# Performance work log

Hardware: AMD Instinct MI355X
Metric: run time of the kernel (lower is better)

The kernel has to match this reference:

```python
import jax, jax.numpy as jnp
import numpy as np

# Multi-scale deformable attention (MSDeformableAttention from RTDETRTransformerv2)
SPATIAL = ((80, 80), (40, 40), (20, 20))  # (h, w) per level, strides 8/16/32 on 640x640
N_HEADS, N_LEVELS, N_POINTS = 8, 3, 4
D_MODEL = 256
HEAD_DIM = D_MODEL // N_HEADS


def setup_inputs() -> dict:
    key = jax.random.key(0)
    ks = jax.random.split(key, 10)
    B, Q = 16, 300
    Lv = sum(h * w for h, w in SPATIAL)  # 8400
    s = 0.02
    return {
        "query": jax.random.normal(ks[0], (B, Q, D_MODEL), jnp.float32),
        "reference_points": jax.random.uniform(ks[1], (B, Q, 4), jnp.float32),
        "value": jax.random.normal(ks[2], (B, Lv, D_MODEL), jnp.float32),
        "Wv": jax.random.normal(ks[3], (D_MODEL, D_MODEL), jnp.float32) * s,
        "bv": jnp.zeros((D_MODEL,), jnp.float32),
        "Woff": jax.random.normal(ks[4], (D_MODEL, N_HEADS * N_LEVELS * N_POINTS * 2), jnp.float32) * s,
        "boff": jax.random.normal(ks[5], (N_HEADS * N_LEVELS * N_POINTS * 2,), jnp.float32) * 0.1,
        "Wattn": jax.random.normal(ks[6], (D_MODEL, N_HEADS * N_LEVELS * N_POINTS), jnp.float32) * s,
        "battn": jnp.zeros((N_HEADS * N_LEVELS * N_POINTS,), jnp.float32),
        "Wout": jax.random.normal(ks[7], (D_MODEL, D_MODEL), jnp.float32) * s,
        "bout": jnp.zeros((D_MODEL,), jnp.float32),
    }


def _grid_sample_level(v_lvl, gx, gy, h, w):
    """Bilinear grid_sample, align_corners=False, zeros padding.

    v_lvl : (B, nH, h*w, hd) flattened per-level value map
    gx,gy : (B, nH, P) sample coords in [-1, 1]
    returns (B, nH, P, hd)
    """
    px = ((gx + 1.0) * w - 1.0) * 0.5  # pixel x
    py = ((gy + 1.0) * h - 1.0) * 0.5  # pixel y
    x0 = jnp.floor(px)
    y0 = jnp.floor(py)
    fx = px - x0
    fy = py - y0
    x0i = x0.astype(jnp.int32)
    y0i = y0.astype(jnp.int32)

    def corner(xi, yi, wgt):
        valid = (xi >= 0) & (xi < w) & (yi >= 0) & (yi < h)
        idx = jnp.clip(yi, 0, h - 1) * w + jnp.clip(xi, 0, w - 1)
        g = jnp.take_along_axis(v_lvl, idx[..., None], axis=2)  # (B,nH,P,hd)
        return g * (wgt * valid.astype(wgt.dtype))[..., None]

    return (corner(x0i, y0i, (1 - fx) * (1 - fy))
            + corner(x0i + 1, y0i, fx * (1 - fy))
            + corner(x0i, y0i + 1, (1 - fx) * fy)
            + corner(x0i + 1, y0i + 1, fx * fy))


def reference(query, reference_points, value, Wv, bv, Woff, boff, Wattn, battn, Wout, bout):
    B, Q, _ = query.shape
    # value projection -> per-head values
    v = (value @ Wv + bv).reshape(B, -1, N_HEADS, HEAD_DIM)
    # sampling offsets and attention weights from queries
    off = (query @ Woff + boff).reshape(B, Q, N_HEADS, N_LEVELS, N_POINTS, 2)
    aw = jax.nn.softmax(
        (query @ Wattn + battn).reshape(B, Q, N_HEADS, N_LEVELS * N_POINTS), axis=-1
    ).reshape(B, Q, N_HEADS, N_LEVELS, N_POINTS)
    # reference points (cx, cy) broadcast over heads/levels/points
    ref = reference_points[:, :, None, None, None, :2]
    pts = jnp.clip(ref + off, 0.0, 1.0)      # (B,Q,nH,nL,nP,2) in [0,1]
    g = pts * 2.0 - 1.0                      # grid_sample coords in [-1,1]

    out = jnp.zeros((B, Q, N_HEADS, HEAD_DIM), query.dtype)
    start = 0
    for lvl, (h, w) in enumerate(SPATIAL):
        v_lvl = v[:, start:start + h * w].transpose(0, 2, 1, 3)  # (B,nH,hw,hd)
        gl = g[:, :, :, lvl]                                     # (B,Q,nH,nP,2)
        gx = gl[..., 0].transpose(0, 2, 1, 3).reshape(B, N_HEADS, Q * N_POINTS)
        gy = gl[..., 1].transpose(0, 2, 1, 3).reshape(B, N_HEADS, Q * N_POINTS)
        sampled = _grid_sample_level(v_lvl, gx, gy, h, w)        # (B,nH,Q*nP,hd)
        sampled = sampled.reshape(B, N_HEADS, Q, N_POINTS, HEAD_DIM)
        wl = aw[:, :, :, lvl].transpose(0, 2, 1, 3)              # (B,nH,Q,nP)
        out = out + jnp.einsum('bhqpd,bhqp->bqhd', sampled, wl)
        start += h * w

    return out.reshape(B, Q, D_MODEL) @ Wout + bout
```

## Files before the change

kernel.cpp:

```cpp
#include <hip/hip_runtime.h>
#include <hip/hip_bf16.h>
#include <cstddef>

#define NB 16
#define NQ 300
#define DM 256
#define LV_ 8400

typedef __attribute__((ext_vector_type(8))) short short8;
typedef __attribute__((ext_vector_type(4))) float f32x4;

static __device__ __forceinline__ unsigned short bf16_rne(float f) {
  unsigned int u = __builtin_bit_cast(unsigned int, f);
  u += 0x7FFFu + ((u >> 16) & 1u);
  return (unsigned short)(u >> 16);
}

static __device__ __forceinline__ unsigned int pack_bf2(float a, float b) {
  __hip_bfloat162 p = __float22bfloat162_rn(make_float2(a, b));
  unsigned int u;
  __builtin_memcpy(&u, &p, 4);
  return u;
}

static __device__ __forceinline__ void gload16(const void* g, void* l) {
  __builtin_amdgcn_global_load_lds(
      (const __attribute__((address_space(1))) unsigned int*)g,
      (__attribute__((address_space(3))) unsigned int*)l, 16, 0, 0);
}

__global__ __launch_bounds__(256) void prep_kernel(
    const float* __restrict__ Wv, const float* __restrict__ Wout,
    unsigned short* __restrict__ WthP, unsigned short* __restrict__ WoutT) {
  __shared__ float tle[32][33];
  const int k0 = blockIdx.x * 32, n0 = blockIdx.y * 32;
  const int xx = threadIdx.x & 31, y4 = (threadIdx.x >> 5) * 4;
  const float* src = blockIdx.z ? Wout : Wv;
  #pragma unroll
  for (int i = 0; i < 4; ++i)
    tle[y4 + i][xx] = src[(size_t)(k0 + y4 + i) * DM + n0 + xx];
  __syncthreads();
  if (blockIdx.z == 0) {
    if (threadIdx.x < 128) {
      const int nl = threadIdx.x >> 2, q8 = threadIdx.x & 3;
      const int n = n0 + nl, yy = n >> 7, col = n & 127;
      uint4 o;
      o.x = pack_bf2(tle[q8 * 8 + 0][nl], tle[q8 * 8 + 1][nl]);
      o.y = pack_bf2(tle[q8 * 8 + 2][nl], tle[q8 * 8 + 3][nl]);
      o.z = pack_bf2(tle[q8 * 8 + 4][nl], tle[q8 * 8 + 5][nl]);
      o.w = pack_bf2(tle[q8 * 8 + 6][nl], tle[q8 * 8 + 7][nl]);
      const size_t idx = ((((size_t)yy * 8 + blockIdx.x) * 4 + q8) * 128 + col) * 8;
      *(uint4*)&WthP[idx] = o;
    }
  } else {
    #pragma unroll
    for (int i = 0; i < 4; ++i)
      WoutT[(size_t)(n0 + y4 + i) * DM + k0 + xx] = bf16_rne(tle[xx][y4 + i]);
  }
}

__global__ __launch_bounds__(256, 3) void vproj_mfma(
    const float* __restrict__ A, const unsigned short* __restrict__ WthP,
    const float* __restrict__ bias, unsigned short* __restrict__ V) {
  __shared__ float Af[2][128][32];
  __shared__ unsigned short Bf[2][4][128][8];
  const int tid = threadIdx.x;
  const int lane = tid & 63;
  const int wave = tid >> 6;
  const int l16 = lane & 15, q4 = lane >> 4;
  const int wr = (wave >> 1) * 64, wc = (wave & 1) * 64;

  const int b = blockIdx.x;
  const int xcd = b & 7, cidx = b >> 3;
  const int w = (xcd < 4 ? xcd * 263 : 4 * 263 + (xcd - 4) * 262) + cidx;
  const int xb = w >> 1, y = w & 1;
  const size_t row0 = (size_t)xb * 128;
  const int col0 = y * 128;

  const unsigned short* bsrc = WthP + (size_t)y * 8 * 4096;

#define STAGE(bufi, kb_) do {                                                  \
    _Pragma("unroll")                                                          \
    for (int c_ = 0; c_ < 4; ++c_) {                                           \
      const int u_ = wave * 4 + c_;                                            \
      const int row_ = u_ * 8 + (lane >> 3);                                   \
      const int lu_ = (lane & 7) ^ (row_ & 7);                                 \
      gload16(A + (row0 + row_) * DM + (kb_) * 32 + lu_ * 4,                   \
              (char*)&Af[bufi][0][0] + u_ * 1024);                             \
    }                                                                          \
    _Pragma("unroll")                                                          \
    for (int c_ = 0; c_ < 2; ++c_) {                                           \
      const int u_ = wave * 2 + c_;                                            \
      gload16(bsrc + (size_t)(kb_) * 4096 + u_ * 512 + lane * 8,               \
              (char*)&Bf[bufi][0][0][0] + u_ * 1024);                          \
    }                                                                          \
  } while (0)

  f32x4 acc[4][4];
  #pragma unroll
  for (int i = 0; i < 4; ++i)
    #pragma unroll
    for (int j = 0; j < 4; ++j) acc[i][j] = (f32x4)0.f;

  int buf = 0;
  STAGE(0, 0);
  __syncthreads();

  for (int kb = 0; kb < 8; ++kb) {
    if (kb < 7) STAGE(buf ^ 1, kb + 1);

    short8 bfr[4];
    #pragma unroll
    for (int j = 0; j < 4; ++j)
      bfr[j] = *(const short8*)&Bf[buf][q4][wc + j * 16 + l16][0];

    #pragma unroll
    for (int i = 0; i < 4; ++i) {
      const int r_ = wr + i * 16 + l16;
      const float* rp = &Af[buf][r_][0];
      const int sw = (r_ & 7);
      const float4 lo = *(const float4*)(rp + ((((q4 << 1) + 0) ^ sw) << 2));
      const float4 hi = *(const float4*)(rp + ((((q4 << 1) + 1) ^ sw) << 2));
      uint4 p;
      p.x = pack_bf2(lo.x, lo.y); p.y = pack_bf2(lo.z, lo.w);
      p.z = pack_bf2(hi.x, hi.y); p.w = pack_bf2(hi.z, hi.w);
      const short8 af = __builtin_bit_cast(short8, p);
      #pragma unroll
      for (int j = 0; j < 4; ++j)
        acc[i][j] = __builtin_amdgcn_mfma_f32_16x16x32_bf16(af, bfr[j], acc[i][j], 0, 0, 0);
    }
    __syncthreads();
    buf ^= 1;
  }
#undef STAGE

  #pragma unroll
  for (int i = 0; i < 4; ++i)
    #pragma unroll
    for (int j = 0; j < 4; ++j) {
      const int col = col0 + wc + j * 16 + l16;
      const float bcol = bias[col];
      #pragma unroll
      for (int r = 0; r < 4; ++r) {
        const size_t row = row0 + wr + i * 16 + q4 * 4 + r;
        V[row * DM + col] = bf16_rne(acc[i][j][r] + bcol);
      }
    }
}

__global__ __launch_bounds__(256) void gemm_qp(
    const float* __restrict__ q,
    const float* __restrict__ Woff, const float* __restrict__ boff,
    const float* __restrict__ Wattn, const float* __restrict__ battn,
    float* __restrict__ offb, float* __restrict__ logitb) {
  const int by = blockIdx.y;
  const float* W; const float* bias; float* C; int N, c0;
  if (by < 6) { W = Woff;  bias = boff;  C = offb;   N = 192; c0 = by * 32; }
  else        { W = Wattn; bias = battn; C = logitb; N = 96;  c0 = (by - 6) * 32; }
  const int m0 = blockIdx.x * 32;

  __shared__ float As[32][33];
  __shared__ float Bs[32][33];
  const int tid = threadIdx.x;
  const int ar = tid >> 3, ak = (tid & 7) * 4;
  const int kr = tid >> 3, bc = (tid & 7) * 4;
  const int tx = tid & 15, ty = tid >> 4;

  const float* apt = q + (size_t)(m0 + ar) * DM + ak;
  float4 av = *(const float4*)apt;
  float4 wv = *(const float4*)(W + (size_t)kr * N + c0 + bc);

  float acc[2][2] = {{0.f, 0.f}, {0.f, 0.f}};
  for (int kk = 0; kk < DM; kk += 32) {
    __syncthreads();
    As[ak + 0][ar] = av.x;
    As[ak + 1][ar] = av.y;
    As[ak + 2][ar] = av.z;
    As[ak + 3][ar] = av.w;
    *(float4*)&Bs[kr][bc] = wv;
    __syncthreads();
    if (kk + 32 < DM) {
      av = *(const float4*)(apt + kk + 32);
      wv = *(const float4*)(W + (size_t)(kk + 32 + kr) * N + c0 + bc);
    }
    #pragma unroll
    for (int k = 0; k < 32; ++k) {
      const float2 a2 = *(const float2*)&As[k][ty * 2];
      const float2 b2 = *(const float2*)&Bs[k][tx * 2];
      acc[0][0] = fmaf(a2.x, b2.x, acc[0][0]);
      acc[0][1] = fmaf(a2.x, b2.y, acc[0][1]);
      acc[1][0] = fmaf(a2.y, b2.x, acc[1][0]);
      acc[1][1] = fmaf(a2.y, b2.y, acc[1][1]);
    }
  }
  const float b0 = bias[c0 + tx * 2], b1 = bias[c0 + tx * 2 + 1];
  #pragma unroll
  for (int i = 0; i < 2; ++i) {
    float2 o; o.x = acc[i][0] + b0; o.y = acc[i][1] + b1;
    *(float2*)&C[(size_t)(m0 + ty * 2 + i) * N + c0 + tx * 2] = o;
  }
}

__global__ __launch_bounds__(512) void sample_kernel(
    const float* __restrict__ refp, const unsigned short* __restrict__ v,
    const float* __restrict__ off, const float* __restrict__ logits,
    unsigned short* __restrict__ mid) {
  const int x = blockIdx.x;
  const int c8 = x & 7, kb = x >> 3;
  const int b = c8 + (kb >= 75 ? 8 : 0);
  const int qp = (kb >= 75 ? kb - 75 : kb);
  const int bq0 = b * NQ + qp * 4;
  const int t = threadIdx.x;
  __shared__ float off_sh[4][192];
  __shared__ float aw_sh[4][96];
  __shared__ int2  iw_sh[4][96][4];
  __shared__ float ref_sh[4][2];

  {
    const float* osrc = off + (size_t)bq0 * 192;
    float* odst = &off_sh[0][0];
    odst[t] = osrc[t];
    if (t < 256) odst[512 + t] = osrc[512 + t];
    const float* lsrc = logits + (size_t)bq0 * 96;
    if (t < 384) (&aw_sh[0][0])[t] = lsrc[t];
    if (t < 8) ref_sh[t >> 1][t & 1] = refp[(bq0 + (t >> 1)) * 4 + (t & 1)];
  }
  __syncthreads();

  if (t < 32) {
    const int q = t >> 3, h = t & 7;
    float* aw = &aw_sh[q][h * 12];
    float m = -1e30f;
    #pragma unroll
    for (int i = 0; i < 12; ++i) m = fmaxf(m, aw[i]);
    float e[12], s = 0.f;
    #pragma unroll
    for (int i = 0; i < 12; ++i) { e[i] = __expf(aw[i] - m); s += e[i]; }
    const float inv = 1.f / s;
    #pragma unroll
    for (int i = 0; i < 12; ++i) aw[i] = e[i] * inv;
  }
  __syncthreads();

  if (t < 384) {
    const int q = t / 96, r = t - q * 96;
    const int h = r / 12, lp = r - h * 12;
    const int l = lp >> 2, p = lp & 3;
    const int LH[3] = {80, 40, 20};
    const int LS[3] = {0, 6400, 8000};
    const int hh = LH[l], ww = LH[l], st = LS[l];
    const int oi = ((h * 3 + l) * 4 + p) * 2;
    const float aw = aw_sh[q][h * 12 + lp];
    const float sx = fminf(fmaxf(ref_sh[q][0] + off_sh[q][oi], 0.f), 1.f);
    const float sy = fminf(fmaxf(ref_sh[q][1] + off_sh[q][oi + 1], 0.f), 1.f);
    const float px = sx * (float)ww - 0.5f;
    const float py = sy * (float)hh - 0.5f;
    const float x0f = floorf(px), y0f = floorf(py);
    const float fx = px - x0f, fy = py - y0f;
    const int x0 = (int)x0f, y0 = (int)y0f;
    const int x1 = x0 + 1, y1 = y0 + 1;
    const bool vx0 = (x0 >= 0) & (x0 < ww), vx1 = (x1 >= 0) & (x1 < ww);
    const bool vy0 = (y0 >= 0) & (y0 < hh), vy1 = (y1 >= 0) & (y1 < hh);
    const int x0c = min(max(x0, 0), ww - 1), x1c = min(max(x1, 0), ww - 1);
    const int y0c = min(max(y0, 0), hh - 1), y1c = min(max(y1, 0), hh - 1);
    const float w0 = aw * (1.f - fx) * (1.f - fy) * ((vx0 & vy0) ? 1.f : 0.f);
    const float w1 = aw * fx * (1.f - fy) * ((vx1 & vy0) ? 1.f : 0.f);
    const float w2 = aw * (1.f - fx) * fy * ((vx0 & vy1) ? 1.f : 0.f);
    const float w3 = aw * fx * fy * ((vx1 & vy1) ? 1.f : 0.f);
    iw_sh[q][r][0] = make_int2(st + y0c * ww + x0c, __float_as_int(w0));
    iw_sh[q][r][1] = make_int2(st + y0c * ww + x1c, __float_as_int(w1));
    iw_sh[q][r][2] = make_int2(st + y1c * ww + x0c, __float_as_int(w2));
    iw_sh[q][r][3] = make_int2(st + y1c * ww + x1c, __float_as_int(w3));
  }
  __syncthreads();

  const int q = t >> 7, h = (t >> 4) & 7, dp = t & 15;
  const unsigned short* vb = v + (size_t)b * LV_ * DM + h * 32 + dp * 2;
  float ax = 0.f, ay = 0.f;
  #pragma unroll
  for (int r = 0; r < 12; ++r) {
    const int rr = h * 12 + r;
    #pragma unroll
    for (int cc = 0; cc < 4; ++cc) {
      const int2 iw = iw_sh[q][rr][cc];
      const float w = __int_as_float(iw.y);
      const unsigned int u = *(const unsigned int*)(vb + (size_t)iw.x * DM);
      ax = fmaf(w, __builtin_bit_cast(float, u << 16), ax);
      ay = fmaf(w, __builtin_bit_cast(float, u & 0xFFFF0000u), ay);
    }
  }
  unsigned short* mp = mid + (size_t)(bq0 + q) * DM + h * 32 + dp * 2;
  *(unsigned int*)mp = pack_bf2(ax, ay);
}

__global__ __launch_bounds__(256) void outp_mfma(
    const unsigned short* __restrict__ midb, const unsigned short* __restrict__ WoutT,
    const float* __restrict__ bias, float* __restrict__ out) {
  __shared__ short Ah[4][64][8];
  __shared__ short Bh[4][64][8];
  const int tid = threadIdx.x;
  const int lane = tid & 63;
  const int wave = tid >> 6;
  const int l16 = lane & 15, q4 = lane >> 4;
  const int wc = wave * 16;
  const int m0 = blockIdx.x * 64, col0 = blockIdx.y * 64;

  const int r = tid >> 2, ch = tid & 3;
  const unsigned short* apt = midb + (size_t)(m0 + r) * DM + ch * 8;
  const unsigned short* wpt = WoutT + (size_t)(col0 + r) * DM + ch * 8;
  uint4 am = *(const uint4*)apt;
  uint4 wm = *(const uint4*)wpt;

  f32x4 acc[4];
  #pragma unroll
  for (int i = 0; i < 4; ++i) acc[i] = (f32x4)0.f;

  for (int kk = 0; kk < DM; kk += 32) {
    __syncthreads();
    *(uint4*)&Ah[ch][r][0] = am;
    *(uint4*)&Bh[ch][r][0] = wm;
    __syncthreads();
    if (kk + 32 < DM) {
      am = *(const uint4*)(apt + kk + 32);
      wm = *(const uint4*)(wpt + kk + 32);
    }
    const short8 bfrag = *(const short8*)&Bh[q4][wc + l16][0];
    #pragma unroll
    for (int i = 0; i < 4; ++i) {
      const short8 af = *(const short8*)&Ah[q4][i * 16 + l16][0];
      acc[i] = __builtin_amdgcn_mfma_f32_16x16x32_bf16(af, bfrag, acc[i], 0, 0, 0);
    }
  }

  const int col = col0 + wc + l16;
  const float bcol = bias[col];
  #pragma unroll
  for (int i = 0; i < 4; ++i)
    #pragma unroll
    for (int rr = 0; rr < 4; ++rr)
      out[(size_t)(m0 + i * 16 + q4 * 4 + rr) * DM + col] = acc[i][rr] + bcol;
}

extern "C" void kernel_launch(void* const* d_in, const int* in_sizes, int n_in,
                              void* d_out, int out_size, void* d_ws, size_t ws_size,
                              hipStream_t stream) {
  (void)in_sizes; (void)n_in; (void)out_size; (void)ws_size;
  const float* query = (const float*)d_in[0];
  const float* refp  = (const float*)d_in[1];
  const float* value = (const float*)d_in[2];
  const float* Wv    = (const float*)d_in[3];
  const float* bv    = (const float*)d_in[4];
  const float* Woff  = (const float*)d_in[5];
  const float* boff  = (const float*)d_in[6];
  const float* Wattn = (const float*)d_in[7];
  const float* battn = (const float*)d_in[8];
  const float* Wout  = (const float*)d_in[9];
  const float* bout  = (const float*)d_in[10];
  float* out = (float*)d_out;

  char* ws = (char*)d_ws;
  unsigned short* v_bf  = (unsigned short*)ws;
  unsigned short* WthP  = (unsigned short*)(ws + 68812800);
  unsigned short* WoutT = (unsigned short*)(ws + 68943872);
  float* offb   = (float*)(ws + 69074944);
  float* logitb = (float*)(ws + 72761344);
  unsigned short* midb = (unsigned short*)(ws + 74604544);

  prep_kernel<<<dim3(8, 8, 2), 256, 0, stream>>>(Wv, Wout, WthP, WoutT);
  gemm_qp<<<dim3(150, 9), 256, 0, stream>>>(query, Woff, boff, Wattn, battn, offb, logitb);
  vproj_mfma<<<2100, 256, 0, stream>>>(value, WthP, bv, v_bf);
  sample_kernel<<<1200, 512, 0, stream>>>(refp, v_bf, offb, logitb, midb);
  outp_mfma<<<dim3(75, 4), 256, 0, stream>>>(midb, WoutT, bout, out);
}
```

Measured before the change: 291.4 us.

## Merge query projection into value-projection launch and vectorize sampling gathers

The separate small-GEMM kernel for offsets and attention logits now runs as extra blocks appended to the value-projection MFMA kernel's grid, reusing its shared memory. This removes one launch and lets the two independent GEMMs overlap. The sampling kernel drops from 512 to 128 threads per block, with each thread gathering 8 bf16 channels via 16-byte loads instead of 2 channels via 4-byte loads. That cuts the number of gather instructions, at the cost of fewer threads available to hide memory latency.

```diff
diff --git a/kernel.cpp b/kernel.cpp
--- a/kernel.cpp
+++ b/kernel.cpp
@@ -21,6 +21,13 @@
   unsigned int u;
   __builtin_memcpy(&u, &p, 4);
   return u;
+}
+
+static __device__ __forceinline__ float bf_lo(unsigned int u) {
+  return __builtin_bit_cast(float, u << 16);
+}
+static __device__ __forceinline__ float bf_hi(unsigned int u) {
+  return __builtin_bit_cast(float, u & 0xFFFF0000u);
 }
 
 static __device__ __forceinline__ void gload16(const void* g, void* l) {
@@ -59,25 +66,31 @@
   }
 }
 
-__global__ __launch_bounds__(256, 3) void vproj_mfma(
+__global__ __launch_bounds__(256, 3) void fused_vg(
     const float* __restrict__ A, const unsigned short* __restrict__ WthP,
-    const float* __restrict__ bias, unsigned short* __restrict__ V) {
+    const float* __restrict__ bias, unsigned short* __restrict__ V,
+    const float* __restrict__ qry,
+    const float* __restrict__ Woff, const float* __restrict__ boff,
+    const float* __restrict__ Wattn, const float* __restrict__ battn,
+    float* __restrict__ offb, float* __restrict__ logitb) {
   __shared__ float Af[2][128][32];
   __shared__ unsigned short Bf[2][4][128][8];
   const int tid = threadIdx.x;
-  const int lane = tid & 63;
-  const int wave = tid >> 6;
-  const int l16 = lane & 15, q4 = lane >> 4;
-  const int wr = (wave >> 1) * 64, wc = (wave & 1) * 64;
-
-  const int b = blockIdx.x;
-  const int xcd = b & 7, cidx = b >> 3;
-  const int w = (xcd < 4 ? xcd * 263 : 4 * 263 + (xcd - 4) * 262) + cidx;
-  const int xb = w >> 1, y = w & 1;
-  const size_t row0 = (size_t)xb * 128;
-  const int col0 = y * 128;
-
-  const unsigned short* bsrc = WthP + (size_t)y * 8 * 4096;
+
+  if (blockIdx.x < 2100) {
+    const int lane = tid & 63;
+    const int wave = tid >> 6;
+    const int l16 = lane & 15, q4 = lane >> 4;
+    const int wr = (wave >> 1) * 64, wc = (wave & 1) * 64;
+
+    const int b = blockIdx.x;
+    const int xcd = b & 7, cidx = b >> 3;
+    const int w = (xcd < 4 ? xcd * 263 : 4 * 263 + (xcd - 4) * 262) + cidx;
+    const int xb = w >> 1, y = w & 1;
+    const size_t row0 = (size_t)xb * 128;
+    const int col0 = y * 128;
+
+    const unsigned short* bsrc = WthP + (size_t)y * 8 * 4096;
 
 #define STAGE(bufi, kb_) do {                                                  \
     _Pragma("unroll")                                                          \
@@ -96,112 +109,109 @@
     }                                                                          \
   } while (0)
 
-  f32x4 acc[4][4];
-  #pragma unroll
-  for (int i = 0; i < 4; ++i)
-    #pragma unroll
-    for (int j = 0; j < 4; ++j) acc[i][j] = (f32x4)0.f;
-
-  int buf = 0;
-  STAGE(0, 0);
-  __syncthreads();
-
-  for (int kb = 0; kb < 8; ++kb) {
-    if (kb < 7) STAGE(buf ^ 1, kb + 1);
-
-    short8 bfr[4];
-    #pragma unroll
-    for (int j = 0; j < 4; ++j)
-      bfr[j] = *(const short8*)&Bf[buf][q4][wc + j * 16 + l16][0];
-
-    #pragma unroll
-    for (int i = 0; i < 4; ++i) {
-      const int r_ = wr + i * 16 + l16;
-      const float* rp = &Af[buf][r_][0];
-      const int sw = (r_ & 7);
-      const float4 lo = *(const float4*)(rp + ((((q4 << 1) + 0) ^ sw) << 2));
-      const float4 hi = *(const float4*)(rp + ((((q4 << 1) + 1) ^ sw) << 2));
-      uint4 p;
-      p.x = pack_bf2(lo.x, lo.y); p.y = pack_bf2(lo.z, lo.w);
-      p.z = pack_bf2(hi.x, hi.y); p.w = pack_bf2(hi.z, hi.w);
-      const short8 af = __builtin_bit_cast(short8, p);
+    f32x4 acc[4][4];
+    #pragma unroll
+    for (int i = 0; i < 4; ++i)
+      #pragma unroll
+      for (int j = 0; j < 4; ++j) acc[i][j] = (f32x4)0.f;
+
+    int buf = 0;
+    STAGE(0, 0);
+    __syncthreads();
+
+    for (int kb = 0; kb < 8; ++kb) {
+      if (kb < 7) STAGE(buf ^ 1, kb + 1);
+
+      short8 bfr[4];
       #pragma unroll
       for (int j = 0; j < 4; ++j)
-        acc[i][j] = __builtin_amdgcn_mfma_f32_16x16x32_bf16(af, bfr[j], acc[i][j], 0, 0, 0);
-    }
-    __syncthreads();
-    buf ^= 1;
-  }
+        bfr[j] = *(const short8*)&Bf[buf][q4][wc + j * 16 + l16][0];
+
+      #pragma unroll
+      for (int i = 0; i < 4; ++i) {
+        const int r_ = wr + i * 16 + l16;
+        const float* rp = &Af[buf][r_][0];
+        const int sw = (r_ & 7);
+        const float4 lo = *(const float4*)(rp + ((((q4 << 1) + 0) ^ sw) << 2));
+        const float4 hi = *(const float4*)(rp + ((((q4 << 1) + 1) ^ sw) << 2));
+        uint4 p;
+        p.x = pack_bf2(lo.x, lo.y); p.y = pack_bf2(lo.z, lo.w);
+        p.z = pack_bf2(hi.x, hi.y); p.w = pack_bf2(hi.z, hi.w);
+        const short8 af = __builtin_bit_cast(short8, p);
+        #pragma unroll
+        for (int j = 0; j < 4; ++j)
+          acc[i][j] = __builtin_amdgcn_mfma_f32_16x16x32_bf16(af, bfr[j], acc[i][j], 0, 0, 0);
+      }
+      __syncthreads();
+      buf ^= 1;
+    }
 #undef STAGE
 
-  #pragma unroll
-  for (int i = 0; i < 4; ++i)
-    #pragma unroll
-    for (int j = 0; j < 4; ++j) {
-      const int col = col0 + wc + j * 16 + l16;
-      const float bcol = bias[col];
-      #pragma unroll
-      for (int r = 0; r < 4; ++r) {
-        const size_t row = row0 + wr + i * 16 + q4 * 4 + r;
-        V[row * DM + col] = bf16_rne(acc[i][j][r] + bcol);
+    #pragma unroll
+    for (int i = 0; i < 4; ++i)
+      #pragma unroll
+      for (int j = 0; j < 4; ++j) {
+        const int col = col0 + wc + j * 16 + l16;
+        const float bcol = bias[col];
+        #pragma unroll
+        for (int r = 0; r < 4; ++r) {
+          const size_t row = row0 + wr + i * 16 + q4 * 4 + r;
+          V[row * DM + col] = bf16_rne(acc[i][j][r] + bcol);
+        }
       }
-    }
-}
-
-__global__ __launch_bounds__(256) void gemm_qp(
-    const float* __restrict__ q,
-    const float* __restrict__ Woff, const float* __restrict__ boff,
-    const float* __restrict__ Wattn, const float* __restrict__ battn,
-    float* __restrict__ offb, float* __restrict__ logitb) {
-  const int by = blockIdx.y;
-  const float* W; const float* bias; float* C; int N, c0;
-  if (by < 6) { W = Woff;  bias = boff;  C = offb;   N = 192; c0 = by * 32; }
-  else        { W = Wattn; bias = battn; C = logitb; N = 96;  c0 = (by - 6) * 32; }
-  const int m0 = blockIdx.x * 32;
-
-  __shared__ float As[32][33];
-  __shared__ float Bs[32][33];
-  const int tid = threadIdx.x;
-  const int ar = tid >> 3, ak = (tid & 7) * 4;
-  const int kr = tid >> 3, bc = (tid & 7) * 4;
-  const int tx = tid & 15, ty = tid >> 4;
-
-  const float* apt = q + (size_t)(m0 + ar) * DM + ak;
-  float4 av = *(const float4*)apt;
-  float4 wv = *(const float4*)(W + (size_t)kr * N + c0 + bc);
-
-  float acc[2][2] = {{0.f, 0.f}, {0.f, 0.f}};
-  for (int kk = 0; kk < DM; kk += 32) {
-    __syncthreads();
-    As[ak + 0][ar] = av.x;
-    As[ak + 1][ar] = av.y;
-    As[ak + 2][ar] = av.z;
-    As[ak + 3][ar] = av.w;
-    *(float4*)&Bs[kr][bc] = wv;
-    __syncthreads();
-    if (kk + 32 < DM) {
-      av = *(const float4*)(apt + kk + 32);
-      wv = *(const float4*)(W + (size_t)(kk + 32 + kr) * N + c0 + bc);
-    }
-    #pragma unroll
-    for (int k = 0; k < 32; ++k) {
-      const float2 a2 = *(const float2*)&As[k][ty * 2];
-      const float2 b2 = *(const float2*)&Bs[k][tx * 2];
-      acc[0][0] = fmaf(a2.x, b2.x, acc[0][0]);
-      acc[0][1] = fmaf(a2.x, b2.y, acc[0][1]);
-      acc[1][0] = fmaf(a2.y, b2.x, acc[1][0]);
-      acc[1][1] = fmaf(a2.y, b2.y, acc[1][1]);
-    }
-  }
-  const float b0 = bias[c0 + tx * 2], b1 = bias[c0 + tx * 2 + 1];
-  #pragma unroll
-  for (int i = 0; i < 2; ++i) {
-    float2 o; o.x = acc[i][0] + b0; o.y = acc[i][1] + b1;
-    *(float2*)&C[(size_t)(m0 + ty * 2 + i) * N + c0 + tx * 2] = o;
-  }
-}
-
-__global__ __launch_bounds__(512) void sample_kernel(
+  } else {
+    const int local = blockIdx.x - 2100;
+    const int bx = local % 150, by = local / 150;
+    const float* W; const float* bb; float* C; int N, c0;
+    if (by < 6) { W = Woff;  bb = boff;  C = offb;   N = 192; c0 = by * 32; }
+    else        { W = Wattn; bb = battn; C = logitb; N = 96;  c0 = (by - 6) * 32; }
+    const int m0 = bx * 32;
+
+    float* shb = &Af[0][0][0];
+    float (*As)[33] = reinterpret_cast<float(*)[33]>(shb);
+    float (*Bs)[33] = reinterpret_cast<float(*)[33]>(shb + 32 * 33);
+
+    const int ar = tid >> 3, ak = (tid & 7) * 4;
+    const int kr = tid >> 3, bc = (tid & 7) * 4;
+    const int tx = tid & 15, ty = tid >> 4;
+
+    const float* apt = qry + (size_t)(m0 + ar) * DM + ak;
+    float4 av = *(const float4*)apt;
+    float4 wv = *(const float4*)(W + (size_t)kr * N + c0 + bc);
+
+    float acc[2][2] = {{0.f, 0.f}, {0.f, 0.f}};
+    for (int kk = 0; kk < DM; kk += 32) {
+      __syncthreads();
+      As[ak + 0][ar] = av.x;
+      As[ak + 1][ar] = av.y;
+      As[ak + 2][ar] = av.z;
+      As[ak + 3][ar] = av.w;
+      *(float4*)&Bs[kr][bc] = wv;
+      __syncthreads();
+      if (kk + 32 < DM) {
+        av = *(const float4*)(apt + kk + 32);
+        wv = *(const float4*)(W + (size_t)(kk + 32 + kr) * N + c0 + bc);
+      }
+      #pragma unroll
+      for (int k = 0; k < 32; ++k) {
+        const float2 a2 = *(const float2*)&As[k][ty * 2];
+        const float2 b2 = *(const float2*)&Bs[k][tx * 2];
+        acc[0][0] = fmaf(a2.x, b2.x, acc[0][0]);
+        acc[0][1] = fmaf(a2.x, b2.y, acc[0][1]);
+        acc[1][0] = fmaf(a2.y, b2.x, acc[1][0]);
+        acc[1][1] = fmaf(a2.y, b2.y, acc[1][1]);
+      }
+    }
+    const float b0 = bb[c0 + tx * 2], b1 = bb[c0 + tx * 2 + 1];
+    #pragma unroll
+    for (int i = 0; i < 2; ++i) {
+      float2 o; o.x = acc[i][0] + b0; o.y = acc[i][1] + b1;
+      *(float2*)&C[(size_t)(m0 + ty * 2 + i) * N + c0 + tx * 2] = o;
+    }
+  }
+}
+
+__global__ __launch_bounds__(128) void sample_kernel(
     const float* __restrict__ refp, const unsigned short* __restrict__ v,
     const float* __restrict__ off, const float* __restrict__ logits,
     unsigned short* __restrict__ mid) {
@@ -219,10 +229,11 @@
   {
     const float* osrc = off + (size_t)bq0 * 192;
     float* odst = &off_sh[0][0];
-    odst[t] = osrc[t];
-    if (t < 256) odst[512 + t] = osrc[512 + t];
+    #pragma unroll
+    for (int i = 0; i < 6; ++i) odst[t + i * 128] = osrc[t + i * 128];
     const float* lsrc = logits + (size_t)bq0 * 96;
-    if (t < 384) (&aw_sh[0][0])[t] = lsrc[t];
+    #pragma unroll
+    for (int i = 0; i < 3; ++i) (&aw_sh[0][0])[t + i * 128] = lsrc[t + i * 128];
     if (t < 8) ref_sh[t >> 1][t & 1] = refp[(bq0 + (t >> 1)) * 4 + (t & 1)];
   }
   __syncthreads();
@@ -242,8 +253,10 @@
   }
   __syncthreads();
 
-  if (t < 384) {
-    const int q = t / 96, r = t - q * 96;
+  #pragma unroll
+  for (int it = 0; it < 3; ++it) {
+    const int tt = t + it * 128;
+    const int q = tt / 96, r = tt - q * 96;
     const int h = r / 12, lp = r - h * 12;
     const int l = lp >> 2, p = lp & 3;
     const int LH[3] = {80, 40, 20};
@@ -274,9 +287,10 @@
   }
   __syncthreads();
 
-  const int q = t >> 7, h = (t >> 4) & 7, dp = t & 15;
-  const unsigned short* vb = v + (size_t)b * LV_ * DM + h * 32 + dp * 2;
-  float ax = 0.f, ay = 0.f;
+  const int q = t >> 5, h = (t >> 2) & 7, c4 = t & 3;
+  const unsigned short* vb = v + (size_t)b * LV_ * DM + h * 32 + c4 * 8;
+  float a0 = 0.f, a1 = 0.f, a2 = 0.f, a3 = 0.f;
+  float a4 = 0.f, a5 = 0.f, a6 = 0.f, a7 = 0.f;
   #pragma unroll
   for (int r = 0; r < 12; ++r) {
     const int rr = h * 12 + r;
@@ -284,13 +298,20 @@
     for (int cc = 0; cc < 4; ++cc) {
       const int2 iw = iw_sh[q][rr][cc];
       const float w = __int_as_float(iw.y);
-      const unsigned int u = *(const unsigned int*)(vb + (size_t)iw.x * DM);
-      ax = fmaf(w, __builtin_bit_cast(float, u << 16), ax);
-      ay = fmaf(w, __builtin_bit_cast(float, u & 0xFFFF0000u), ay);
-    }
-  }
-  unsigned short* mp = mid + (size_t)(bq0 + q) * DM + h * 32 + dp * 2;
-  *(unsigned int*)mp = pack_bf2(ax, ay);
+      const uint4 u = *(const uint4*)(vb + (size_t)iw.x * DM);
+      a0 = fmaf(w, bf_lo(u.x), a0); a1 = fmaf(w, bf_hi(u.x), a1);
+      a2 = fmaf(w, bf_lo(u.y), a2); a3 = fmaf(w, bf_hi(u.y), a3);
+      a4 = fmaf(w, bf_lo(u.z), a4); a5 = fmaf(w, bf_hi(u.z), a5);
+      a6 = fmaf(w, bf_lo(u.w), a6); a7 = fmaf(w, bf_hi(u.w), a7);
+    }
+  }
+  unsigned short* mp = mid + (size_t)(bq0 + q) * DM + h * 32 + c4 * 8;
+  uint4 o;
+  o.x = pack_bf2(a0, a1);
+  o.y = pack_bf2(a2, a3);
+  o.z = pack_bf2(a4, a5);
+  o.w = pack_bf2(a6, a7);
+  *(uint4*)mp = o;
 }
 
 __global__ __launch_bounds__(256) void outp_mfma(
@@ -367,8 +388,9 @@
   unsigned short* midb = (unsigned short*)(ws + 74604544);
 
   prep_kernel<<<dim3(8, 8, 2), 256, 0, stream>>>(Wv, Wout, WthP, WoutT);
-  gemm_qp<<<dim3(150, 9), 256, 0, stream>>>(query, Woff, boff, Wattn, battn, offb, logitb);
-  vproj_mfma<<<2100, 256, 0, stream>>>(value, WthP, bv, v_bf);
-  sample_kernel<<<1200, 512, 0, stream>>>(refp, v_bf, offb, logitb, midb);
+  fused_vg<<<3450, 256, 0, stream>>>(value, WthP, bv, v_bf,
+                                     query, Woff, boff, Wattn, battn,
+                                     offb, logitb);
+  sample_kernel<<<1200, 128, 0, stream>>>(refp, v_bf, offb, logitb, midb);
   outp_mfma<<<dim3(75, 4), 256, 0, stream>>>(midb, WoutT, bout, out);
 }
```

New measurement: 422.8 us. 1.45x slower.
